# Performance work log

Measured on AMD Instinct MI355X. Metric: run time of the kernel, lower is better.

The kernel has to match this reference:

```python
import jax, jax.numpy as jnp
import numpy as np

EPS = 1e-5

def _bn(x, gamma, beta):
    # training-mode BatchNorm1d over the batch axis (axis=1 of (K,B,H)), biased variance
    m = jnp.mean(x, axis=1, keepdims=True)
    v = jnp.mean((x - m) ** 2, axis=1, keepdims=True)
    return (x - m) * jax.lax.rsqrt(v + EPS) * gamma[:, None, :] + beta[:, None, :]

def setup_inputs() -> dict:
    key = jax.random.key(0)
    ks = jax.random.split(key, 20)
    B, T, D, H, K = 4096, 64, 256, 128, 12
    data_x = jax.random.randint(ks[0], (B, T, 1), 0, 2, dtype=jnp.int32)
    feats = jax.random.normal(ks[1], (B, T + 1, D), dtype=jnp.float32)
    s = 0.05
    return {
        "data_x": data_x,
        "feats": feats,
        "w_atom": jax.random.normal(ks[2], (K, D), jnp.float32) * s,
        "b_atom": jnp.zeros((K,), jnp.float32),
        "W1": jax.random.normal(ks[3], (K, D, H), jnp.float32) * s,
        "b1": jnp.zeros((K, H), jnp.float32),
        "g1": jnp.ones((K, H), jnp.float32),
        "be1": jnp.zeros((K, H), jnp.float32),
        "W2": jax.random.normal(ks[4], (K, H, H), jnp.float32) * s,
        "b2": jnp.zeros((K, H), jnp.float32),
        "g2": jnp.ones((K, H), jnp.float32),
        "be2": jnp.zeros((K, H), jnp.float32),
        "W3": jax.random.normal(ks[5], (K, H, H), jnp.float32) * s,
        "b3": jnp.zeros((K, H), jnp.float32),
        "g3": jnp.ones((K, H), jnp.float32),
        "be3": jnp.zeros((K, H), jnp.float32),
        "Wout": jax.random.normal(ks[6], (K, H), jnp.float32) * s,
        "bout": jnp.zeros((K,), jnp.float32),
    }

def reference(data_x, feats, w_atom, b_atom, W1, b1, g1, be1, W2, b2, g2, be2, W3, b3, g3, be3, Wout, bout):
    # valid-node mask: padding where data_x[:,:,0]==0
    valid = (data_x[:, :, 0] != 0).astype(feats.dtype)          # (B,T)
    f = feats[:, 1:, :]                                          # (B,T,D)
    # per-task atom importance weights (sigmoid(Linear(D,1)))
    w = jax.nn.sigmoid(jnp.einsum('btd,kd->kbt', f, w_atom) + b_atom[:, None, None])  # (K,B,T)
    # weighted segment-sum readout per molecule (sum_nodes with weight 'w' over valid atoms)
    mol = jnp.einsum('kbt,bt,btd->kbd', w, valid, f)             # (K,B,D)
    # per-task MLP heads: Dropout(0)->Linear->ReLU->BatchNorm1d, x3, then Linear(H,1)
    h1 = _bn(jax.nn.relu(jnp.einsum('kbd,kdh->kbh', mol, W1) + b1[:, None, :]), g1, be1)
    h2 = _bn(jax.nn.relu(jnp.einsum('kbh,khj->kbj', h1, W2) + b2[:, None, :]), g2, be2)
    h3 = _bn(jax.nn.relu(jnp.einsum('kbh,khj->kbj', h2, W3) + b3[:, None, :]), g3, be3)
    pred = jnp.einsum('kbh,kh->kb', h3, Wout) + bout[:, None]    # (K,B)
    prediction_all = pred.T                                      # (B,K) = torch.cat over tasks
    atom_weights = w * valid[None, :, :]                         # (K,B,T), dense-padded atom weight list
    return (prediction_all, atom_weights)
```

## Files before the change

### kernel.cpp

```cpp
#include <hip/hip_runtime.h>
#include <hip/hip_bf16.h>

#define B_N 4096
#define T_N 64
#define D_N 256
#define H_N 128
#define K_N 12

typedef __attribute__((ext_vector_type(8))) short short8;
typedef __attribute__((ext_vector_type(4))) float f32x4;

static __device__ __forceinline__ unsigned bf16_rne(float x) {
  unsigned u = __float_as_uint(x);
  return (u + 0x7fffu + ((u >> 16) & 1u)) >> 16;
}
static __device__ __forceinline__ unsigned pk2(float a, float b) {
  return bf16_rne(a) | (bf16_rne(b) << 16);
}
static __device__ __forceinline__ float lo16(unsigned u) { return __uint_as_float(u << 16); }
static __device__ __forceinline__ float hi16(unsigned u) { return __uint_as_float(u & 0xffff0000u); }

__device__ __forceinline__ void pack_w(const float* W, unsigned* out, int S, int id) {
  const int lane = id & 63;
  const int s  = (id >> 6) % S;
  const int nt = ((id >> 6) / S) & 7;
  const int kk = id / (64 * S * 8);
  const int n  = nt * 16 + (lane & 15);
  const int d0 = 32 * s + 8 * (lane >> 4);
  const int D  = 32 * S;
  unsigned o[4];
#pragma unroll
  for (int j = 0; j < 4; ++j) {
    const float a = W[(size_t)kk * D * H_N + (d0 + 2 * j) * H_N + n];
    const float b = W[(size_t)kk * D * H_N + (d0 + 2 * j + 1) * H_N + n];
    o[j] = pk2(a, b);
  }
  *(uint4*)(out + (size_t)id * 4) = make_uint4(o[0], o[1], o[2], o[3]);
}

__global__ void prep_all(const float* __restrict__ w_atom,
                         const float* __restrict__ W1, const float* __restrict__ W2,
                         const float* __restrict__ W3,
                         unsigned* __restrict__ wa_frag, unsigned* __restrict__ w1p,
                         unsigned* __restrict__ w2p, unsigned* __restrict__ w3p,
                         float* __restrict__ st)
{
  const int bid = blockIdx.x, tid = threadIdx.x;
  if (bid < 2) {
    const int id = bid * 256 + tid;
    const int s = id >> 6, l = id & 63;
    const int k = l & 15, h = l >> 4, d0 = s * 32 + h * 8;
    unsigned o[4];
#pragma unroll
    for (int j = 0; j < 4; ++j) {
      const float a = (k < K_N) ? w_atom[k * D_N + d0 + 2 * j]     : 0.f;
      const float b = (k < K_N) ? w_atom[k * D_N + d0 + 2 * j + 1] : 0.f;
      o[j] = pk2(a, b);
    }
    *(uint4*)(wa_frag + (size_t)id * 4) = make_uint4(o[0], o[1], o[2], o[3]);
  } else if (bid < 194) {
    pack_w(W1, w1p, 8, (bid - 2) * 256 + tid);
  } else if (bid < 290) {
    pack_w(W2, w2p, 4, (bid - 194) * 256 + tid);
  } else if (bid < 386) {
    pack_w(W3, w3p, 4, (bid - 290) * 256 + tid);
  } else {
    const int id = (bid - 386) * 256 + tid;
    if (id < 9216) st[id] = 0.f;
  }
}

__global__ __launch_bounds__(256, 4) void k1_mol(
    const int* __restrict__ dx, const float* __restrict__ feats,
    const unsigned* __restrict__ wa_frag, const float* __restrict__ b_atom,
    float* __restrict__ out_atom, unsigned short* __restrict__ mol16)
{
  __shared__ unsigned tile[64 * 128];
  __shared__ float wv32[16 * 68];

  const int tid  = threadIdx.x;
  const int lane = tid & 63;
  const int w    = tid >> 6;
  const int b    = blockIdx.x;
  const int k    = lane & 15;
  const int h    = lane >> 4;

  short8 bfr[8];
  {
    const short8* wf8 = (const short8*)wa_frag;
#pragma unroll
    for (int s = 0; s < 8; ++s) bfr[s] = wf8[s * 64 + lane];
  }
  const float ba = (k < K_N) ? b_atom[k] : 0.f;
  const int4 dvv = *(const int4*)(dx + b * T_N + 16 * w + 4 * h);

  wv32[816 + tid] = 0.f;
  if (tid < 16) wv32[1072 + tid] = 0.f;

  const float* fg = feats + ((size_t)b * 65 + 1) * 256;
#pragma unroll
  for (int c = 0; c < 4; ++c) {
    float4 v[4];
#pragma unroll
    for (int i = 0; i < 4; ++i)
      v[i] = *(const float4*)(fg + (size_t)(16 * w + 4 * c + i) * 256 + 4 * lane);
#pragma unroll
    for (int i = 0; i < 4; ++i) {
      const int tl = 4 * c + i;
      const int t  = 16 * w + tl;
      const unsigned off = t * 128 + (((lane >> 1) ^ tl) << 2) + (lane & 1) * 2;
      *(uint2*)&tile[off] = make_uint2(pk2(v[i].x, v[i].y), pk2(v[i].z, v[i].w));
    }
  }

  f32x4 cacc = {0.f, 0.f, 0.f, 0.f};
#pragma unroll
  for (int s = 0; s < 8; ++s) {
    const unsigned off = (16 * w + k) * 128 + (((4 * s + h) ^ k) << 2);
    const short8 afrag = *(const short8*)&tile[off];
    cacc = __builtin_amdgcn_mfma_f32_16x16x32_bf16(afrag, bfr[s], cacc, 0, 0, 0);
  }

#pragma unroll
  for (int r = 0; r < 4; ++r) {
    const float valid = (((const int*)&dvv)[r] != 0) ? 1.f : 0.f;
    const float wv = valid / (1.f + __expf(-(cacc[r] + ba)));
    if (k < K_N) wv32[k * 68 + 16 * w + 4 * h + r] = wv;
  }
  __syncthreads();

  const unsigned short* tile_u16 = (const unsigned short*)tile;
  f32x4 c2[4];
#pragma unroll
  for (int j = 0; j < 4; ++j) c2[j] = (f32x4){0.f, 0.f, 0.f, 0.f};

#pragma unroll
  for (int s = 0; s < 2; ++s) {
    const float4 a0 = *(const float4*)&wv32[k * 68 + 32 * s + 8 * h];
    const float4 a1 = *(const float4*)&wv32[k * 68 + 32 * s + 8 * h + 4];
    union { unsigned u[4]; short8 s8; } au;
    au.u[0] = pk2(a0.x, a0.y); au.u[1] = pk2(a0.z, a0.w);
    au.u[2] = pk2(a1.x, a1.y); au.u[3] = pk2(a1.z, a1.w);

#pragma unroll
    for (int j = 0; j < 4; ++j) {
      const int dd = (4 * w + j) * 16 + k;
      const int g  = dd >> 3;
      const int dl = dd & 7;
      union { unsigned short us[8]; short8 s8; } bu;
#pragma unroll
      for (int jj = 0; jj < 8; ++jj) {
        const int t = 32 * s + 8 * h + jj;
        bu.us[jj] = tile_u16[(t << 8) + (((g ^ (t & 15))) << 3) + dl];
      }
      c2[j] = __builtin_amdgcn_mfma_f32_16x16x32_bf16(au.s8, bu.s8, c2[j], 0, 0, 0);
    }
  }

  if (h < 3) {
#pragma unroll
    for (int j = 0; j < 4; ++j) {
#pragma unroll
      for (int r = 0; r < 4; ++r) {
        const int kk = 4 * h + r;
        mol16[((size_t)kk * B_N + b) * 256 + (4 * w + j) * 16 + k] =
            (unsigned short)bf16_rne(c2[j][r]);
      }
    }
  }

  if (tid < 192) {
    const int kk = tid >> 4, t0 = (tid & 15) * 4;
    const float4 v = *(const float4*)&wv32[kk * 68 + t0];
    *(float4*)&out_atom[((size_t)kk * B_N + b) * T_N + t0] = v;
  }
}

template <int S, bool AFFINE>
__global__ __launch_bounds__(256) void gemm_mfma(
    const unsigned* __restrict__ Abf, const unsigned* __restrict__ wpack,
    const float* __restrict__ bias,
    const float* __restrict__ ssum_p, const float* __restrict__ ssq_p,
    const float* __restrict__ g_p, const float* __restrict__ be_p,
    unsigned short* __restrict__ Hout,
    float* __restrict__ ssum, float* __restrict__ ssq)
{
  __shared__ unsigned tile[64 * S * 16];
  __shared__ float redS[4][8][16];
  __shared__ float redQ[4][8][16];
  __shared__ float alds[H_N], blds[H_N];

  const int k   = blockIdx.y;
  const int b0  = blockIdx.x << 6;
  const int tid = threadIdx.x;
  const int lane = tid & 63;
  const int wv  = tid >> 6;
  const int ln15 = lane & 15;
  const int hq   = lane >> 4;

  if (AFFINE) {
    if (tid < H_N) {
      const float inv_n = 1.f / (float)B_N;
      const float m = ssum_p[k * H_N + tid] * inv_n;
      float v = fmaf(ssq_p[k * H_N + tid], inv_n, -m * m);
      v = fmaxf(v, 0.f);
      const float a = g_p[k * H_N + tid] * rsqrtf(v + 1e-5f);
      alds[tid] = a;
      blds[tid] = fmaf(-m, a, be_p[k * H_N + tid]);
    }
    __syncthreads();
  }

  {
    const int row = tid >> 2, q = tid & 3;
    const uint4* Ar = (const uint4*)Abf + ((size_t)k * B_N + b0 + row) * (S * 4) + q * S;
#pragma unroll
    for (int gi = 0; gi < S; ++gi) {
      const int g = q * S + gi;
      uint4 u = Ar[gi];
      if (AFFINE) {
        const float4 al0 = *(const float4*)(alds + g * 8);
        const float4 al1 = *(const float4*)(alds + g * 8 + 4);
        const float4 bt0 = *(const float4*)(blds + g * 8);
        const float4 bt1 = *(const float4*)(blds + g * 8 + 4);
        u.x = pk2(fmaf(lo16(u.x), al0.x, bt0.x), fmaf(hi16(u.x), al0.y, bt0.y));
        u.y = pk2(fmaf(lo16(u.y), al0.z, bt0.z), fmaf(hi16(u.y), al0.w, bt0.w));
        u.z = pk2(fmaf(lo16(u.z), al1.x, bt1.x), fmaf(hi16(u.z), al1.y, bt1.y));
        u.w = pk2(fmaf(lo16(u.w), al1.z, bt1.z), fmaf(hi16(u.w), al1.w, bt1.w));
      }
      *(uint4*)&tile[row * (S * 16) + ((g ^ (row & 15)) << 2)] = u;
    }
  }
  __syncthreads();

  const short8* wp8 = (const short8*)wpack + (size_t)k * 8 * S * 64 + lane;
  f32x4 acc[8];
#pragma unroll
  for (int nt = 0; nt < 8; ++nt) acc[nt] = (f32x4){0.f, 0.f, 0.f, 0.f};

  short8 bs0[8], bs1[8];
#pragma unroll
  for (int nt = 0; nt < 8; ++nt) bs0[nt] = wp8[(nt * S) * 64];
#pragma unroll
  for (int s = 0; s < S; ++s) {
    if (s + 1 < S) {
#pragma unroll
      for (int nt = 0; nt < 8; ++nt) {
        if (s & 1) bs0[nt] = wp8[(nt * S + s + 1) * 64];
        else       bs1[nt] = wp8[(nt * S + s + 1) * 64];
      }
    }
    const int arow = (wv << 4) + ln15;
    const unsigned aoff = arow * (S * 16) + (((4 * s + hq) ^ ln15) << 2);
    const short8 af = *(const short8*)&tile[aoff];
#pragma unroll
    for (int nt = 0; nt < 8; ++nt) {
      const short8 bf = (s & 1) ? bs1[nt] : bs0[nt];
      acc[nt] = __builtin_amdgcn_mfma_f32_16x16x32_bf16(af, bf, acc[nt], 0, 0, 0);
    }
  }

#pragma unroll
  for (int nt = 0; nt < 8; ++nt) {
    const int col = nt * 16 + ln15;
    const float bv = bias[k * H_N + col];
    float cs = 0.f, cq = 0.f;
#pragma unroll
    for (int r = 0; r < 4; ++r) {
      const float o = fmaxf(acc[nt][r] + bv, 0.f);
      cs += o; cq = fmaf(o, o, cq);
      const int row = b0 + (wv << 4) + (hq << 2) + r;
      Hout[((size_t)k * B_N + row) * H_N + col] = (unsigned short)bf16_rne(o);
    }
    cs += __shfl_xor(cs, 16); cs += __shfl_xor(cs, 32);
    cq += __shfl_xor(cq, 16); cq += __shfl_xor(cq, 32);
    if (lane < 16) { redS[wv][nt][ln15] = cs; redQ[wv][nt][ln15] = cq; }
  }
  __syncthreads();
  if (tid < 128) {
    const int nt = tid >> 4, c = tid & 15;
    float s = 0.f, q = 0.f;
#pragma unroll
    for (int i = 0; i < 4; ++i) { s += redS[i][nt][c]; q += redQ[i][nt][c]; }
    atomicAdd(&ssum[k * H_N + nt * 16 + c], s);
    atomicAdd(&ssq[k * H_N + nt * 16 + c], q);
  }
}

__global__ __launch_bounds__(256) void k_pred(
    const unsigned* __restrict__ h3,
    const float* __restrict__ s3, const float* __restrict__ q3,
    const float* __restrict__ g3, const float* __restrict__ be3,
    const float* __restrict__ Wout, const float* __restrict__ bout,
    float* __restrict__ out)
{
  const int lane = threadIdx.x & 63;
  const int wv   = threadIdx.x >> 6;
  const int pair = blockIdx.x * 4 + wv;
  const int b = pair / K_N, k = pair - b * K_N;
  const int i0 = k * H_N + (lane << 1);

  const float inv_n = 1.f / (float)B_N;
  const float2 sv = *(const float2*)(s3 + i0);
  const float2 qv = *(const float2*)(q3 + i0);
  const float2 gv = *(const float2*)(g3 + i0);
  const float2 bev = *(const float2*)(be3 + i0);
  const float mx = sv.x * inv_n, my = sv.y * inv_n;
  const float vx = fmaxf(fmaf(qv.x, inv_n, -mx * mx), 0.f);
  const float vy = fmaxf(fmaf(qv.y, inv_n, -my * my), 0.f);
  const float ax = gv.x * rsqrtf(vx + 1e-5f);
  const float ay = gv.y * rsqrtf(vy + 1e-5f);
  const float bx = fmaf(-mx, ax, bev.x);
  const float by = fmaf(-my, ay, bev.y);

  const unsigned xp = h3[((size_t)k * B_N + b) * 64 + lane];
  const float2 wo = *(const float2*)(Wout + i0);
  float s = fmaf(lo16(xp), ax, bx) * wo.x + fmaf(hi16(xp), ay, by) * wo.y;
#pragma unroll
  for (int off = 32; off; off >>= 1) s += __shfl_down(s, off);
  if (lane == 0) out[pair] = s + bout[k];
}

extern "C" void kernel_launch(void* const* d_in, const int* in_sizes, int n_in,
                              void* d_out, int out_size, void* d_ws, size_t ws_size,
                              hipStream_t stream)
{
  (void)in_sizes; (void)n_in; (void)out_size; (void)ws_size;
  const int*   dx     = (const int*)d_in[0];
  const float* feats  = (const float*)d_in[1];
  const float* w_atom = (const float*)d_in[2];
  const float* b_atom = (const float*)d_in[3];
  const float* W1 = (const float*)d_in[4];
  const float* b1 = (const float*)d_in[5];
  const float* g1 = (const float*)d_in[6];
  const float* be1 = (const float*)d_in[7];
  const float* W2 = (const float*)d_in[8];
  const float* b2 = (const float*)d_in[9];
  const float* g2 = (const float*)d_in[10];
  const float* be2 = (const float*)d_in[11];
  const float* W3 = (const float*)d_in[12];
  const float* b3 = (const float*)d_in[13];
  const float* g3 = (const float*)d_in[14];
  const float* be3 = (const float*)d_in[15];
  const float* Wout = (const float*)d_in[16];
  const float* bout = (const float*)d_in[17];

  float* out      = (float*)d_out;
  float* pred_out = out;
  float* atom_out = out + (size_t)B_N * K_N;

  char* wsb = (char*)d_ws;
  unsigned short* mol16 = (unsigned short*)wsb;
  unsigned short* h1   = (unsigned short*)(wsb + 25165824);
  unsigned short* h2   = (unsigned short*)(wsb + 37748736);
  unsigned short* h3   = (unsigned short*)(wsb + 50331648);
  float* st = (float*)(wsb + 62914560);
  float* s1 = st,        *q1 = st + 1536;
  float* s2 = st + 3072, *q2 = st + 4608;
  float* s3 = st + 6144, *q3 = st + 7680;
  unsigned* wa_frag = (unsigned*)(st + 9216);
  unsigned* w1p = wa_frag + 2048;
  unsigned* w2p = w1p + 196608;
  unsigned* w3p = w2p + 98304;

  prep_all<<<422, 256, 0, stream>>>(w_atom, W1, W2, W3, wa_frag, w1p, w2p, w3p, st);

  k1_mol<<<B_N, 256, 0, stream>>>(dx, feats, wa_frag, b_atom, atom_out, mol16);

  gemm_mfma<8, false><<<dim3(64, 12), 256, 0, stream>>>(
      (const unsigned*)mol16, w1p, b1, nullptr, nullptr, nullptr, nullptr, h1, s1, q1);
  gemm_mfma<4, true><<<dim3(64, 12), 256, 0, stream>>>(
      (const unsigned*)h1, w2p, b2, s1, q1, g1, be1, h2, s2, q2);
  gemm_mfma<4, true><<<dim3(64, 12), 256, 0, stream>>>(
      (const unsigned*)h2, w3p, b3, s2, q2, g2, be2, h3, s3, q3);
  k_pred<<<B_N * K_N / 4, 256, 0, stream>>>(
      (const unsigned*)h3, s3, q3, g3, be3, Wout, bout, pred_out);
}
```

Measured before the change: 125.5 us.

## Restructure k1_mol to 128 threads with half-tile staging and FMA weighted readout

```diff
diff --git a/kernel.cpp b/kernel.cpp
--- a/kernel.cpp
+++ b/kernel.cpp
@@ -70,13 +70,13 @@
   }
 }
 
-__global__ __launch_bounds__(256, 4) void k1_mol(
+__global__ __launch_bounds__(128, 4) void k1_mol(
     const int* __restrict__ dx, const float* __restrict__ feats,
     const unsigned* __restrict__ wa_frag, const float* __restrict__ b_atom,
     float* __restrict__ out_atom, unsigned short* __restrict__ mol16)
 {
-  __shared__ unsigned tile[64 * 128];
-  __shared__ float wv32[16 * 68];
+  __shared__ unsigned tile[32 * 128];
+  __shared__ float wv32[K_N * 68];
 
   const int tid  = threadIdx.x;
   const int lane = tid & 63;
@@ -92,85 +92,82 @@
     for (int s = 0; s < 8; ++s) bfr[s] = wf8[s * 64 + lane];
   }
   const float ba = (k < K_N) ? b_atom[k] : 0.f;
-  const int4 dvv = *(const int4*)(dx + b * T_N + 16 * w + 4 * h);
-
-  wv32[816 + tid] = 0.f;
-  if (tid < 16) wv32[1072 + tid] = 0.f;
 
   const float* fg = feats + ((size_t)b * 65 + 1) * 256;
-#pragma unroll
-  for (int c = 0; c < 4; ++c) {
-    float4 v[4];
-#pragma unroll
-    for (int i = 0; i < 4; ++i)
-      v[i] = *(const float4*)(fg + (size_t)(16 * w + 4 * c + i) * 256 + 4 * lane);
-#pragma unroll
-    for (int i = 0; i < 4; ++i) {
-      const int tl = 4 * c + i;
-      const int t  = 16 * w + tl;
-      const unsigned off = t * 128 + (((lane >> 1) ^ tl) << 2) + (lane & 1) * 2;
-      *(uint2*)&tile[off] = make_uint2(pk2(v[i].x, v[i].y), pk2(v[i].z, v[i].w));
-    }
-  }
-
-  f32x4 cacc = {0.f, 0.f, 0.f, 0.f};
-#pragma unroll
-  for (int s = 0; s < 8; ++s) {
-    const unsigned off = (16 * w + k) * 128 + (((4 * s + h) ^ k) << 2);
-    const short8 afrag = *(const short8*)&tile[off];
-    cacc = __builtin_amdgcn_mfma_f32_16x16x32_bf16(afrag, bfr[s], cacc, 0, 0, 0);
-  }
-
-#pragma unroll
-  for (int r = 0; r < 4; ++r) {
-    const float valid = (((const int*)&dvv)[r] != 0) ? 1.f : 0.f;
-    const float wv = valid / (1.f + __expf(-(cacc[r] + ba)));
-    if (k < K_N) wv32[k * 68 + 16 * w + 4 * h + r] = wv;
-  }
-  __syncthreads();
-
-  const unsigned short* tile_u16 = (const unsigned short*)tile;
-  f32x4 c2[4];
-#pragma unroll
-  for (int j = 0; j < 4; ++j) c2[j] = (f32x4){0.f, 0.f, 0.f, 0.f};
-
-#pragma unroll
-  for (int s = 0; s < 2; ++s) {
-    const float4 a0 = *(const float4*)&wv32[k * 68 + 32 * s + 8 * h];
-    const float4 a1 = *(const float4*)&wv32[k * 68 + 32 * s + 8 * h + 4];
-    union { unsigned u[4]; short8 s8; } au;
-    au.u[0] = pk2(a0.x, a0.y); au.u[1] = pk2(a0.z, a0.w);
-    au.u[2] = pk2(a1.x, a1.y); au.u[3] = pk2(a1.z, a1.w);
-
-#pragma unroll
-    for (int j = 0; j < 4; ++j) {
-      const int dd = (4 * w + j) * 16 + k;
-      const int g  = dd >> 3;
-      const int dl = dd & 7;
-      union { unsigned short us[8]; short8 s8; } bu;
-#pragma unroll
-      for (int jj = 0; jj < 8; ++jj) {
-        const int t = 32 * s + 8 * h + jj;
-        bu.us[jj] = tile_u16[(t << 8) + (((g ^ (t & 15))) << 3) + dl];
+
+  float4 m[6];
+#pragma unroll
+  for (int kk = 0; kk < 6; ++kk) m[kk] = make_float4(0.f, 0.f, 0.f, 0.f);
+  const int kb = 6 * w;
+
+#pragma unroll
+  for (int H = 0; H < 2; ++H) {
+    if (H) __syncthreads();
+
+#pragma unroll
+    for (int c = 0; c < 4; ++c) {
+      float4 v[4];
+#pragma unroll
+      for (int i = 0; i < 4; ++i)
+        v[i] = *(const float4*)(fg + (size_t)(32 * H + 16 * w + 4 * c + i) * 256 + 4 * lane);
+#pragma unroll
+      for (int i = 0; i < 4; ++i) {
+        const int tl = 4 * c + i;
+        const int rl = 16 * w + tl;
+        const unsigned off = rl * 128 + (((lane >> 1) ^ (rl & 15)) << 2) + (lane & 1) * 2;
+        *(uint2*)&tile[off] = make_uint2(pk2(v[i].x, v[i].y), pk2(v[i].z, v[i].w));
       }
-      c2[j] = __builtin_amdgcn_mfma_f32_16x16x32_bf16(au.s8, bu.s8, c2[j], 0, 0, 0);
-    }
-  }
-
-  if (h < 3) {
-#pragma unroll
-    for (int j = 0; j < 4; ++j) {
-#pragma unroll
-      for (int r = 0; r < 4; ++r) {
-        const int kk = 4 * h + r;
-        mol16[((size_t)kk * B_N + b) * 256 + (4 * w + j) * 16 + k] =
-            (unsigned short)bf16_rne(c2[j][r]);
+    }
+
+    f32x4 cacc = {0.f, 0.f, 0.f, 0.f};
+#pragma unroll
+    for (int s = 0; s < 8; ++s) {
+      const unsigned off = (16 * w + k) * 128 + (((4 * s + h) ^ k) << 2);
+      const short8 afrag = *(const short8*)&tile[off];
+      cacc = __builtin_amdgcn_mfma_f32_16x16x32_bf16(afrag, bfr[s], cacc, 0, 0, 0);
+    }
+
+    const int4 dvv = *(const int4*)(dx + b * T_N + 32 * H + 16 * w + 4 * h);
+#pragma unroll
+    for (int r = 0; r < 4; ++r) {
+      const float valid = (((const int*)&dvv)[r] != 0) ? 1.f : 0.f;
+      const float wv = valid / (1.f + __expf(-(cacc[r] + ba)));
+      if (k < K_N) wv32[k * 68 + 32 * H + 16 * w + 4 * h + r] = wv;
+    }
+    __syncthreads();
+
+#pragma unroll
+    for (int tc = 0; tc < 8; ++tc) {
+      float4 wvv[6];
+#pragma unroll
+      for (int kk = 0; kk < 6; ++kk)
+        wvv[kk] = *(const float4*)&wv32[(kb + kk) * 68 + 32 * H + (tc << 2)];
+#pragma unroll
+      for (int j = 0; j < 4; ++j) {
+        const int rl = (tc << 2) + j;
+        const unsigned off = rl * 128 + (((lane >> 1) ^ (rl & 15)) << 2) + (lane & 1) * 2;
+        const uint2 pw = *(const uint2*)&tile[off];
+        const float f0 = lo16(pw.x), f1 = hi16(pw.x);
+        const float f2 = lo16(pw.y), f3 = hi16(pw.y);
+#pragma unroll
+        for (int kk = 0; kk < 6; ++kk) {
+          const float wj = ((const float*)&wvv[kk])[j];
+          m[kk].x = fmaf(wj, f0, m[kk].x); m[kk].y = fmaf(wj, f1, m[kk].y);
+          m[kk].z = fmaf(wj, f2, m[kk].z); m[kk].w = fmaf(wj, f3, m[kk].w);
+        }
       }
     }
   }
 
-  if (tid < 192) {
-    const int kk = tid >> 4, t0 = (tid & 15) * 4;
+#pragma unroll
+  for (int kk = 0; kk < 6; ++kk) {
+    unsigned short* mp = mol16 + ((size_t)(kb + kk) * B_N + b) * 256 + 4 * lane;
+    *(uint2*)mp = make_uint2(pk2(m[kk].x, m[kk].y), pk2(m[kk].z, m[kk].w));
+  }
+
+#pragma unroll
+  for (int i = tid; i < 192; i += 128) {
+    const int kk = i >> 4, t0 = (i & 15) * 4;
     const float4 v = *(const float4*)&wv32[kk * 68 + t0];
     *(float4*)&out_atom[((size_t)kk * B_N + b) * T_N + t0] = v;
   }
@@ -365,7 +362,7 @@
 
   prep_all<<<422, 256, 0, stream>>>(w_atom, W1, W2, W3, wa_frag, w1p, w2p, w3p, st);
 
-  k1_mol<<<B_N, 256, 0, stream>>>(dx, feats, wa_frag, b_atom, atom_out, mol16);
+  k1_mol<<<B_N, 128, 0, stream>>>(dx, feats, wa_frag, b_atom, atom_out, mol16);
 
   gemm_mfma<8, false><<<dim3(64, 12), 256, 0, stream>>>(
       (const unsigned*)mol16, w1p, b1, nullptr, nullptr, nullptr, nullptr, h1, s1, q1);
```

After: 207.4 us. 1.65x slower.
